# Kernel optimization log

Measured on AMD Instinct MI355X. Metric: run time of the kernel, lower is better.

## Reference

```python
import jax, jax.numpy as jnp
import numpy as np

N, E, G = 32768, 262144, 512
IN_DIM, HID, HEADS = 300, 128, 4
D_FUSED = HID * HEADS  # 512
L = 3


def setup_inputs() -> dict:
    key = jax.random.key(0)
    ks = jax.random.split(key, 24)
    s = 0.02
    inp = {
        "x": jax.random.normal(ks[0], (N, IN_DIM), jnp.float32),
        "edge_index": jax.random.randint(ks[1], (2, E), 0, N, jnp.int32),
        "batch": jnp.sort(jax.random.randint(ks[2], (N,), 0, G, jnp.int32)),
        "syn_w": jax.random.normal(ks[3], (IN_DIM, HID)) * s,
        "syn_b": jnp.zeros((HID,), jnp.float32),
        "ant_w": jax.random.normal(ks[4], (IN_DIM, HID)) * s,
        "ant_b": jnp.zeros((HID,), jnp.float32),
        "fusion_w": jax.random.normal(ks[5], (2 * HID, D_FUSED)) * s,
        "fusion_b": jnp.zeros((D_FUSED,), jnp.float32),
        "Wq": jax.random.normal(ks[6], (L, D_FUSED, D_FUSED)) * s,
        "bq": jnp.zeros((L, D_FUSED), jnp.float32),
        "Wk": jax.random.normal(ks[7], (L, D_FUSED, D_FUSED)) * s,
        "bk": jnp.zeros((L, D_FUSED), jnp.float32),
        "Wv": jax.random.normal(ks[8], (L, D_FUSED, D_FUSED)) * s,
        "bv": jnp.zeros((L, D_FUSED), jnp.float32),
        "Wskip": jax.random.normal(ks[9], (L, D_FUSED, D_FUSED)) * s,
        "bskip": jnp.zeros((L, D_FUSED), jnp.float32),
        "cls_w1": jax.random.normal(ks[10], (D_FUSED, HID)) * s,
        "cls_b1": jnp.zeros((HID,), jnp.float32),
        "cls_w2": jax.random.normal(ks[11], (HID, 1)) * s,
        "cls_b2": jnp.zeros((1,), jnp.float32),
    }
    return inp


def _transformer_conv(h, src, dst, Wq, bq, Wk, bk, Wv, bv, Wskip, bskip):
    # PyG TransformerConv: per-edge dot-product attention, softmax over in-neighbors of dst,
    # concat heads, plus root/skip linear (root_weight=True, concat=True, no edge_attr).
    n = h.shape[0]
    q = (h @ Wq + bq).reshape(n, HEADS, HID)
    k = (h @ Wk + bk).reshape(n, HEADS, HID)
    v = (h @ Wv + bv).reshape(n, HEADS, HID)
    scale = 1.0 / np.sqrt(HID)
    logits = jnp.einsum("ehd,ehd->eh", q[dst], k[src]) * scale  # [E, H]
    m = jax.ops.segment_max(logits, dst, num_segments=n)        # [N, H]
    e = jnp.exp(logits - m[dst])
    z = jax.ops.segment_sum(e, dst, num_segments=n)
    alpha = e / (z[dst] + 1e-16)                                # [E, H]
    msg = alpha[:, :, None] * v[src]                            # [E, H, D]
    out = jax.ops.segment_sum(msg, dst, num_segments=n).reshape(n, D_FUSED)
    return out + h @ Wskip + bskip


def reference(x, edge_index, batch, syn_w, syn_b, ant_w, ant_b, fusion_w, fusion_b,
              Wq, bq, Wk, bk, Wv, bv, Wskip, bskip, cls_w1, cls_b1, cls_w2, cls_b2):
    x_syn = jax.nn.relu(x @ syn_w + syn_b)
    x_ant = jax.nn.relu(x @ ant_w + ant_b)
    h = jnp.concatenate([x_syn, x_ant], axis=1) @ fusion_w + fusion_b  # [N, 512]
    src, dst = edge_index[0], edge_index[1]
    for l in range(L):
        h = jax.nn.relu(_transformer_conv(h, src, dst, Wq[l], bq[l], Wk[l], bk[l],
                                          Wv[l], bv[l], Wskip[l], bskip[l]))
    cnt = jax.ops.segment_sum(jnp.ones((h.shape[0],), h.dtype), batch, num_segments=G)
    pooled = jax.ops.segment_sum(h, batch, num_segments=G) / jnp.maximum(cnt, 1.0)[:, None]
    hid = jax.nn.relu(pooled @ cls_w1 + cls_b1)
    out = jax.nn.sigmoid(hid @ cls_w2 + cls_b2)
    return out.squeeze()
```

## Files before the change

kernel.cpp:

```cpp
#include <hip/hip_runtime.h>
#include <hip/hip_bf16.h>
#include <hip/hip_fp8.h>
#include <math.h>

#define N_NODES 32768
#define N_EDGES 262144
#define N_GRAPHS 512
#define IN_DIM 300
#define KPAD 320
#define HID 128
#define HEADS 4
#define D_FUSED 512
#define N_LAYERS 3

typedef __hip_bfloat16 bf16;
typedef short bf16x8 __attribute__((ext_vector_type(8)));
typedef float f32x4 __attribute__((ext_vector_type(4)));
typedef float f32x2 __attribute__((ext_vector_type(2)));

__device__ __forceinline__ float bfs_to_f(short s)
{
    unsigned u = ((unsigned)(unsigned short)s) << 16;
    return __builtin_bit_cast(float, u);
}

__device__ __forceinline__ short f_to_bfs(float v)
{
    return (short)__builtin_bit_cast(unsigned short, __float2bfloat16(v));
}

__device__ __forceinline__ void bf8_to_f32(bf16x8 v, float* f)
{
#pragma unroll
    for (int j = 0; j < 8; ++j) f[j] = bfs_to_f(v[j]);
}

__device__ __forceinline__ unsigned char f32_to_fp8(float v)
{
#if __has_builtin(__builtin_amdgcn_cvt_pk_fp8_f32)
    int p = __builtin_amdgcn_cvt_pk_fp8_f32(v, v, 0, false);
    return (unsigned char)(p & 0xff);
#else
    __hip_fp8_e4m3 t(v);
    return (unsigned char)t.__x;
#endif
}

__device__ __forceinline__ void fp8x8_to_f32(uint2 w, float* f)
{
#if __has_builtin(__builtin_amdgcn_cvt_pk_f32_fp8)
    f32x2 a = __builtin_amdgcn_cvt_pk_f32_fp8((int)w.x, false);
    f32x2 b = __builtin_amdgcn_cvt_pk_f32_fp8((int)w.x, true);
    f32x2 c = __builtin_amdgcn_cvt_pk_f32_fp8((int)w.y, false);
    f32x2 d = __builtin_amdgcn_cvt_pk_f32_fp8((int)w.y, true);
    f[0] = a.x; f[1] = a.y; f[2] = b.x; f[3] = b.y;
    f[4] = c.x; f[5] = c.y; f[6] = d.x; f[7] = d.y;
#else
    const unsigned char* p = (const unsigned char*)&w;
#pragma unroll
    for (int j = 0; j < 8; ++j) {
        __hip_fp8_e4m3 t;
        t.__x = (__hip_fp8_storage_t)p[j];
        f[j] = (float)t;
    }
#endif
}

__device__ __forceinline__ void gload_lds16(const void* g, void* l)
{
    __builtin_amdgcn_global_load_lds(
        (const __attribute__((address_space(1))) void*)g,
        (__attribute__((address_space(3))) void*)l, 16, 0, 0);
}

template <int K, int ACT, int EPI>
__global__ __launch_bounds__(512, 2) void mfma_gemm256(
    const bf16* __restrict__ A, int lda,
    const bf16* __restrict__ Bt,
    const float* __restrict__ bias,
    bf16* __restrict__ C0, int ldc0,
    bf16* __restrict__ C1, int ldc1, int csplit,
    unsigned char* __restrict__ C2,
    int nbx)
{
    __shared__ __align__(16) char lds[131072];

    const int t = threadIdx.x;
    const int wid = t >> 6, lane = t & 63;
    const int hi = lane >> 4, li = lane & 15;
    const int wr = wid >> 2, wc = wid & 3;

    int wg = blockIdx.x;
    if ((gridDim.x & 7) == 0) {
        const int cpx = gridDim.x >> 3;
        wg = (wg & 7) * cpx + (wg >> 3);
    }
    const int mb = wg / nbx, nb = wg % nbx;
    const int brow = mb * 256, bcol = nb * 256;
    constexpr int NT = K >> 6;

    const bf16* gA[4];
    const bf16* gB[4];
    int lbA[4], lbB[4];
#pragma unroll
    for (int j = 0; j < 4; ++j) {
        const int c = j * 512 + wid * 64 + lane;
        const int row = c >> 3;
        const int colb8 = ((c & 7) ^ (row & 7)) * 8;
        gA[j] = A + (size_t)(brow + row) * lda + colb8;
        gB[j] = Bt + (size_t)(bcol + row) * K + colb8;
        lbA[j] = (j * 512 + wid * 64) * 16;
        lbB[j] = 32768 + (j * 512 + wid * 64) * 16;
    }

    f32x4 acc[8][4] = {};

    auto stage = [&](int buf, int kt) {
        const int ko = kt * 64;
#pragma unroll
        for (int j = 0; j < 4; ++j)
            gload_lds16(gA[j] + ko, lds + buf * 65536 + lbA[j]);
#pragma unroll
        for (int j = 0; j < 4; ++j)
            gload_lds16(gB[j] + ko, lds + buf * 65536 + lbB[j]);
    };

    auto compute = [&](int b) {
        const char* Ab = lds + b * 65536;
        const char* Bb = Ab + 32768;
        bf16x8 bfrag[4][2];
#pragma unroll
        for (int n = 0; n < 4; ++n)
#pragma unroll
            for (int ks = 0; ks < 2; ++ks) {
                const int row = wc * 64 + n * 16 + li;
                bfrag[n][ks] = *(const bf16x8*)(
                    Bb + row * 128 + (((ks * 4 + hi) ^ (row & 7)) << 4));
            }
#pragma unroll
        for (int p = 0; p < 4; ++p) {
            bf16x8 afrag[2][2];
#pragma unroll
            for (int mm = 0; mm < 2; ++mm)
#pragma unroll
                for (int ks = 0; ks < 2; ++ks) {
                    const int row = wr * 128 + (p * 2 + mm) * 16 + li;
                    afrag[mm][ks] = *(const bf16x8*)(
                        Ab + row * 128 + (((ks * 4 + hi) ^ (row & 7)) << 4));
                }
            __builtin_amdgcn_s_setprio(1);
#pragma unroll
            for (int ks = 0; ks < 2; ++ks)
#pragma unroll
                for (int mm = 0; mm < 2; ++mm)
#pragma unroll
                    for (int n = 0; n < 4; ++n)
                        acc[p * 2 + mm][n] = __builtin_amdgcn_mfma_f32_16x16x32_bf16(
                            afrag[mm][ks], bfrag[n][ks], acc[p * 2 + mm][n], 0, 0, 0);
            __builtin_amdgcn_s_setprio(0);
        }
    };

    stage(0, 0);
#pragma unroll
    for (int kt = 0; kt < NT - 1; ++kt) {
        const int b = kt & 1;
        stage(b ^ 1, kt + 1);
        asm volatile("s_waitcnt vmcnt(8)" ::: "memory");
        __builtin_amdgcn_s_barrier();
        compute(b);
        asm volatile("" ::: "memory");
        __builtin_amdgcn_s_barrier();
    }
    asm volatile("s_waitcnt vmcnt(0)" ::: "memory");
    __builtin_amdgcn_s_barrier();
    compute((NT - 1) & 1);

#pragma unroll
    for (int m = 0; m < 8; ++m) {
#pragma unroll
        for (int n = 0; n < 4; ++n) {
            const int col = bcol + wc * 64 + n * 16 + li;
            const float bv = bias[col];
            if (EPI == 0) {
                const bool lo = (col < csplit);
                bf16* Cd = lo ? C0 : C1;
                const int ldc = lo ? ldc0 : ldc1;
                const int cc = lo ? col : col - csplit;
#pragma unroll
                for (int r = 0; r < 4; ++r) {
                    const int row = brow + wr * 128 + m * 16 + hi * 4 + r;
                    float v = acc[m][n][r] + bv;
                    if (ACT == 1) v = fmaxf(v, 0.f);
                    Cd[(size_t)row * ldc + cc] = __float2bfloat16(v);
                }
            } else {
#pragma unroll
                for (int r = 0; r < 4; ++r) {
                    const int row = brow + wr * 128 + m * 16 + hi * 4 + r;
                    const float v = acc[m][n][r] + bv;
                    if (col < 512) {
                        C0[(size_t)row * ldc0 + col] = __float2bfloat16(v);
                    } else if (col < 1024) {
                        C1[(size_t)row * ldc1 + (col - 512)] = __float2bfloat16(v);
                    } else {
                        C2[(size_t)row * 1024 + (col - 1024)] = f32_to_fp8(v);
                    }
                }
            }
        }
    }
}

template <int ACT>
__global__ __launch_bounds__(256) void mfma_gemm(
    const bf16* __restrict__ A, int lda,
    const bf16* __restrict__ Bt,
    const float* __restrict__ bias,
    bf16* __restrict__ C, int ldc, int K)
{
    __shared__ __align__(16) char lds[16384];
    char* As = lds;
    char* Bs = lds + 8192;

    const int t = threadIdx.x;
    const int wid = t >> 6, lane = t & 63;
    const int brow = blockIdx.x * 128;
    const int bcol = blockIdx.y * 128;
    const int wr = wid >> 1, wc = wid & 1;

    f32x4 acc[4][4] = {};

    for (int k0 = 0; k0 < K; k0 += 32) {
#pragma unroll
        for (int j = 0; j < 2; ++j) {
            const int seg = wid * 2 + j;
            const int row = seg * 16 + (lane >> 2);
            const int clin = lane & 3;
            const int clog = clin ^ ((row >> 1) & 3);
            gload_lds16(A + (size_t)(brow + row) * lda + k0 + clog * 8,
                        As + seg * 1024);
            gload_lds16(Bt + (size_t)(bcol + row) * K + k0 + clog * 8,
                        Bs + seg * 1024);
        }
        __syncthreads();

        bf16x8 af[4], bfr[4];
#pragma unroll
        for (int m = 0; m < 4; ++m) {
            const int row = wr * 64 + m * 16 + (lane & 15);
            const int cl = (lane >> 4) ^ ((row >> 1) & 3);
            af[m] = *(const bf16x8*)(As + row * 64 + cl * 16);
        }
#pragma unroll
        for (int n = 0; n < 4; ++n) {
            const int row = wc * 64 + n * 16 + (lane & 15);
            const int cl = (lane >> 4) ^ ((row >> 1) & 3);
            bfr[n] = *(const bf16x8*)(Bs + row * 64 + cl * 16);
        }
#pragma unroll
        for (int m = 0; m < 4; ++m)
#pragma unroll
            for (int n = 0; n < 4; ++n)
                acc[m][n] = __builtin_amdgcn_mfma_f32_16x16x32_bf16(
                    af[m], bfr[n], acc[m][n], 0, 0, 0);
        __syncthreads();
    }

#pragma unroll
    for (int m = 0; m < 4; ++m) {
#pragma unroll
        for (int n = 0; n < 4; ++n) {
            const int col = bcol + wc * 64 + n * 16 + (lane & 15);
            const float bv = bias[col];
#pragma unroll
            for (int r = 0; r < 4; ++r) {
                const int row = brow + wr * 64 + m * 16 + (lane >> 4) * 4 + r;
                float v = acc[m][n][r] + bv;
                if (ACT == 1) v = fmaxf(v, 0.f);
                C[(size_t)row * ldc + col] = __float2bfloat16(v);
            }
        }
    }
}

__global__ void prep_xpad_kernel(const float* __restrict__ x, bf16* __restrict__ xb)
{
    const int n = blockIdx.x, k = threadIdx.x;
    xb[(size_t)n * KPAD + k] =
        __float2bfloat16(k < IN_DIM ? x[(size_t)n * IN_DIM + k] : 0.f);
}

__global__ void prep_encw_kernel(const float* __restrict__ syn_w,
                                 const float* __restrict__ ant_w,
                                 bf16* __restrict__ wt)
{
    const int c = blockIdx.x, k = threadIdx.x;
    float v = 0.f;
    if (k < IN_DIM) v = (c < HID) ? syn_w[k * HID + c] : ant_w[k * HID + (c - HID)];
    wt[c * KPAD + k] = __float2bfloat16(v);
}

__global__ void prep_fusw_kernel(const float* __restrict__ fw, bf16* __restrict__ wt)
{
    const int c = blockIdx.x, k = threadIdx.x;
    wt[c * 256 + k] = __float2bfloat16(fw[k * D_FUSED + c]);
}

__global__ __launch_bounds__(256) void prep_combw_kernel(
    const float* __restrict__ Wskip,
    const float* __restrict__ Wq,
    const float* __restrict__ Wk,
    const float* __restrict__ Wv,
    bf16* __restrict__ wt)
{
    __shared__ float tile[32][33];
    const int blk = blockIdx.x;
    const int l = blk >> 10, rem = blk & 1023;
    const int cb = rem >> 4, kb = rem & 15;
    const int c0 = cb * 32;

    const int sel = c0 >> 9;
    const float* mat = (sel == 0) ? Wskip : (sel == 1) ? Wq : (sel == 2) ? Wk : Wv;
    const int cp0 = c0 & 511;

    const int j = threadIdx.x & 31;
    const int i0 = threadIdx.x >> 5;
#pragma unroll
    for (int s = 0; s < 4; ++s) {
        const int i = i0 + 8 * s;
        tile[i][j] = mat[((size_t)l * 512 + kb * 32 + i) * 512 + cp0 + j];
    }
    __syncthreads();
#pragma unroll
    for (int s = 0; s < 4; ++s) {
        const int jj = i0 + 8 * s;
        wt[((size_t)l * 2048 + c0 + jj) * 512 + kb * 32 + j] =
            __float2bfloat16(tile[j][jj]);
    }
}

__global__ void prep_bias_kernel(const float* __restrict__ syn_b,
                                 const float* __restrict__ ant_b,
                                 const float* __restrict__ bskip,
                                 const float* __restrict__ bq,
                                 const float* __restrict__ bk,
                                 const float* __restrict__ bv,
                                 float* __restrict__ benc,
                                 float* __restrict__ bcomb)
{
    const int i = blockIdx.x * 256 + threadIdx.x;
    if (i < 256) benc[i] = (i < HID) ? syn_b[i] : ant_b[i - HID];
    const int j = i - 256;
    if (j >= 0 && j < 6144) {
        const int l = j >> 11, c = j & 2047;
        const int sel = c >> 9, col = c & 511;
        const float* s = (sel == 0) ? bskip : (sel == 1) ? bq : (sel == 2) ? bk : bv;
        bcomb[j] = s[l * D_FUSED + col];
    }
}

__global__ void zero_int_kernel(int* __restrict__ p, int n)
{
    int i = blockIdx.x * 256 + threadIdx.x;
    if (i < n) p[i] = 0;
}

__global__ void hist_kernel(const int* __restrict__ dst, int* __restrict__ deg, int E)
{
    int e = blockIdx.x * 256 + threadIdx.x;
    if (e < E) atomicAdd(&deg[dst[e]], 1);
}

__global__ __launch_bounds__(256) void partial_sum_kernel(const int* __restrict__ deg,
                                                          int* __restrict__ part)
{
    int v = deg[blockIdx.x * 256 + threadIdx.x];
#pragma unroll
    for (int o = 32; o; o >>= 1) v += __shfl_xor(v, o);
    __shared__ int w4[4];
    if ((threadIdx.x & 63) == 0) w4[threadIdx.x >> 6] = v;
    __syncthreads();
    if (threadIdx.x == 0) part[blockIdx.x] = w4[0] + w4[1] + w4[2] + w4[3];
}

__global__ __launch_bounds__(128) void scan_part_kernel(int* __restrict__ part)
{
    __shared__ int s[128];
    const int t = threadIdx.x;
    s[t] = part[t];
    __syncthreads();
    for (int o = 1; o < 128; o <<= 1) {
        int v = (t >= o) ? s[t - o] : 0;
        __syncthreads();
        s[t] += v;
        __syncthreads();
    }
    part[t] = (t == 0) ? 0 : s[t - 1];
}

__global__ __launch_bounds__(256) void off_kernel(const int* __restrict__ deg,
                                                  const int* __restrict__ part,
                                                  int* __restrict__ off)
{
    __shared__ int s[256];
    const int b = blockIdx.x, t = threadIdx.x;
    s[t] = deg[b * 256 + t];
    __syncthreads();
    for (int o = 1; o < 256; o <<= 1) {
        int v = (t >= o) ? s[t - o] : 0;
        __syncthreads();
        s[t] += v;
        __syncthreads();
    }
    const int excl = (t == 0) ? 0 : s[t - 1];
    off[b * 256 + t] = part[b] + excl;
    if (b == 127 && t == 255) off[N_NODES] = part[127] + s[255];
}

__global__ void scatter_kernel(const int* __restrict__ src, const int* __restrict__ dst,
                               const int* __restrict__ off, int* __restrict__ cursor,
                               int* __restrict__ csr_src, int E)
{
    int e = blockIdx.x * 256 + threadIdx.x;
    if (e < E) {
        int d = dst[e];
        int pos = atomicAdd(&cursor[d], 1);
        csr_src[off[d] + pos] = src[e];
    }
}

__global__ __launch_bounds__(256) void attn_kernel(
    const bf16* __restrict__ qb, const unsigned char* __restrict__ kvb,
    bf16* __restrict__ hout, const int* __restrict__ off,
    const int* __restrict__ csr)
{
    const int n = blockIdx.x;
    const int hd = threadIdx.x >> 6;
    const int lane = threadIdx.x & 63;
    const int g = lane >> 4, sub = lane & 15;
    const float scale = 0.08838834764831845f;

    float qf[8];
    bf8_to_f32(*(const bf16x8*)(qb + (size_t)n * 512 + hd * 128 + sub * 8), qf);

    float m = -1e30f, z = 0.f;
    float acc[8] = {};

    const int s0 = off[n], s1 = off[n + 1];
    for (int e0 = s0; e0 < s1; e0 += 4) {
        const int e = e0 + g;
        const bool valid = (e < s1);
        const int srcn = valid ? csr[e] : 0;
        const unsigned char* kp = kvb + (size_t)srcn * 1024 + hd * 128 + sub * 8;

        float kf[8];
        fp8x8_to_f32(*(const uint2*)kp, kf);
        float d = 0.f;
#pragma unroll
        for (int j = 0; j < 8; ++j) d = fmaf(qf[j], kf[j], d);
        d += __shfl_xor(d, 1);
        d += __shfl_xor(d, 2);
        d += __shfl_xor(d, 4);
        d += __shfl_xor(d, 8);

        const float logit = d * scale;
        const float mn = valid ? fmaxf(m, logit) : m;
        const float corr = __expf(m - mn);
        const float w = valid ? __expf(logit - mn) : 0.f;
        z = z * corr + w;

        float vf[8];
        fp8x8_to_f32(*(const uint2*)(kp + 512), vf);
#pragma unroll
        for (int j = 0; j < 8; ++j) acc[j] = acc[j] * corr + w * vf[j];
        m = mn;
    }

    float mm = fmaxf(m, __shfl_xor(m, 16));
    mm = fmaxf(mm, __shfl_xor(mm, 32));
    const float f = __expf(m - mm);
    float zz = z * f;
    zz += __shfl_xor(zz, 16);
    zz += __shfl_xor(zz, 32);
    const float inv = 1.f / (zz + 1e-16f);

    float o[8];
#pragma unroll
    for (int j = 0; j < 8; ++j) {
        float a = acc[j] * f;
        a += __shfl_xor(a, 16);
        a += __shfl_xor(a, 32);
        o[j] = a * inv;
    }

    if (g == 0) {
        const size_t ob = (size_t)n * D_FUSED + hd * HID + sub * 8;
        const bf16x8 sk = *(const bf16x8*)(hout + ob);
        bf16x8 res;
#pragma unroll
        for (int j = 0; j < 8; ++j)
            res[j] = f_to_bfs(fmaxf(o[j] + bfs_to_f(sk[j]), 0.f));
        *(bf16x8*)(hout + ob) = res;
    }
}

__global__ __launch_bounds__(256) void pool_kernel(const bf16* __restrict__ h,
                                                   const int* __restrict__ batch,
                                                   float* __restrict__ pooled)
{
    const int g = blockIdx.x;
    int a = 0, b = N_NODES;
    while (a < b) { int mid = (a + b) >> 1; if (batch[mid] < g) a = mid + 1; else b = mid; }
    const int start = a;
    b = N_NODES;
    while (a < b) { int mid = (a + b) >> 1; if (batch[mid] < g + 1) a = mid + 1; else b = mid; }
    const int end = a;
    const float invc = 1.f / fmaxf((float)(end - start), 1.f);

    const int t = threadIdx.x;
    float2 s = make_float2(0.f, 0.f);
    for (int nidx = start; nidx < end; ++nidx) {
        const bf16* p = h + (size_t)nidx * D_FUSED + t * 2;
        s.x += bfs_to_f(((const short*)p)[0]);
        s.y += bfs_to_f(((const short*)p)[1]);
    }
    pooled[(size_t)g * D_FUSED + t * 2]     = s.x * invc;
    pooled[(size_t)g * D_FUSED + t * 2 + 1] = s.y * invc;
}

__global__ __launch_bounds__(128) void cls_kernel(const float* __restrict__ pooled,
                                                  const float* __restrict__ w1,
                                                  const float* __restrict__ b1,
                                                  const float* __restrict__ w2,
                                                  const float* __restrict__ b2,
                                                  float* __restrict__ out)
{
    const int g = blockIdx.x;
    const int j = threadIdx.x;
    const float* p = pooled + (size_t)g * D_FUSED;
    float acc = 0.f;
    for (int i = 0; i < D_FUSED; ++i) acc += p[i] * w1[i * HID + j];
    const float hid = fmaxf(acc + b1[j], 0.f);
    float val = hid * w2[j];
#pragma unroll
    for (int o = 32; o; o >>= 1) val += __shfl_xor(val, o);
    __shared__ float ws2[2];
    if ((threadIdx.x & 63) == 0) ws2[threadIdx.x >> 6] = val;
    __syncthreads();
    if (threadIdx.x == 0) {
        const float sum = ws2[0] + ws2[1] + b2[0];
        out[g] = 1.f / (1.f + __expf(-sum));
    }
}

extern "C" void kernel_launch(void* const* d_in, const int* in_sizes, int n_in,
                              void* d_out, int out_size, void* d_ws, size_t ws_size,
                              hipStream_t stream)
{
    const float* x        = (const float*)d_in[0];
    const int*   ei       = (const int*)d_in[1];
    const int*   batch    = (const int*)d_in[2];
    const float* syn_w    = (const float*)d_in[3];
    const float* syn_b    = (const float*)d_in[4];
    const float* ant_w    = (const float*)d_in[5];
    const float* ant_b    = (const float*)d_in[6];
    const float* fusion_w = (const float*)d_in[7];
    const float* fusion_b = (const float*)d_in[8];
    const float* Wq       = (const float*)d_in[9];
    const float* bq       = (const float*)d_in[10];
    const float* Wk       = (const float*)d_in[11];
    const float* bk       = (const float*)d_in[12];
    const float* Wv       = (const float*)d_in[13];
    const float* bv       = (const float*)d_in[14];
    const float* Wskip    = (const float*)d_in[15];
    const float* bskip    = (const float*)d_in[16];
    const float* cls_w1   = (const float*)d_in[17];
    const float* cls_b1   = (const float*)d_in[18];
    const float* cls_w2   = (const float*)d_in[19];
    const float* cls_b2   = (const float*)d_in[20];

    const int* src = ei;
    const int* dst = ei + N_EDGES;

    const size_t NV = (size_t)N_NODES * D_FUSED;
    bf16* hA    = (bf16*)d_ws;
    bf16* hB    = hA + NV;
    bf16* qbuf  = hB + NV;
    unsigned char* kvbuf = (unsigned char*)(qbuf + NV);
    bf16* wenc  = (bf16*)(kvbuf + (size_t)N_NODES * 1024);
    bf16* wfus  = wenc + 256 * KPAD;
    bf16* wcomb = wfus + 512 * 256;
    float* benc = (float*)(wcomb + (size_t)3 * 2048 * 512);
    float* bcomb = benc + 256;
    float* pooled = bcomb + 6144;
    int* deg    = (int*)(pooled + (size_t)N_GRAPHS * D_FUSED);
    int* cursor = deg + N_NODES;
    int* part   = cursor + N_NODES;
    int* off    = part + 128;
    int* csr    = off + N_NODES + 1;

    bf16* xb   = qbuf;
    bf16* tenc = hB;

    zero_int_kernel<<<(2 * N_NODES + 255) / 256, 256, 0, stream>>>(deg, 2 * N_NODES);
    hist_kernel<<<N_EDGES / 256, 256, 0, stream>>>(dst, deg, N_EDGES);
    partial_sum_kernel<<<128, 256, 0, stream>>>(deg, part);
    scan_part_kernel<<<1, 128, 0, stream>>>(part);
    off_kernel<<<128, 256, 0, stream>>>(deg, part, off);
    scatter_kernel<<<N_EDGES / 256, 256, 0, stream>>>(src, dst, off, cursor, csr, N_EDGES);

    prep_xpad_kernel<<<N_NODES, KPAD, 0, stream>>>(x, xb);
    prep_encw_kernel<<<256, KPAD, 0, stream>>>(syn_w, ant_w, wenc);
    prep_fusw_kernel<<<512, 256, 0, stream>>>(fusion_w, wfus);
    prep_combw_kernel<<<3072, 256, 0, stream>>>(Wskip, Wq, Wk, Wv, wcomb);
    prep_bias_kernel<<<25, 256, 0, stream>>>(syn_b, ant_b, bskip, bq, bk, bv, benc, bcomb);

    mfma_gemm<1><<<dim3(N_NODES / 128, 2), 256, 0, stream>>>(
        xb, KPAD, wenc, benc, tenc, 256, KPAD);
    mfma_gemm256<256, 0, 0><<<256, 512, 0, stream>>>(
        tenc, 256, wfus, fusion_b, hA, D_FUSED, hA, D_FUSED, D_FUSED, nullptr, 2);

    bf16* hcur = hA;
    bf16* hnew = hB;
    for (int l = 0; l < N_LAYERS; ++l) {
        mfma_gemm256<512, 0, 1><<<1024, 512, 0, stream>>>(
            hcur, D_FUSED, wcomb + (size_t)l * 2048 * D_FUSED,
            bcomb + (size_t)l * 2048,
            hnew, D_FUSED, qbuf, D_FUSED, 512, kvbuf, 8);
        attn_kernel<<<N_NODES, 256, 0, stream>>>(qbuf, kvbuf, hnew, off, csr);
        bf16* tmp = hcur; hcur = hnew; hnew = tmp;
    }

    pool_kernel<<<N_GRAPHS, 256, 0, stream>>>(hcur, batch, pooled);
    cls_kernel<<<N_GRAPHS, 128, 0, stream>>>(pooled, cls_w1, cls_b1, cls_w2, cls_b2,
                                             (float*)d_out);
}
```

Baseline: 647.6 us.

## Interleave next-tile global-to-LDS loads with MFMA phases in GEMM main loop

Restructures the 256x256 bf16 GEMM main loop so the prefetch of the next K tile is split into four parts, each issued between the MFMA phases of the current tile. Barriers are added around each phase, and the LDS layout is reorganized into 128-row slabs. The goal is to spread memory traffic across the compute and keep the issue pattern balanced, in the style of ping-pong scheduling. The extra barriers per phase add synchronization cost and could stall waves.

Result: no change. 654.3 us (+1.0%).

```diff
diff --git a/kernel.cpp b/kernel.cpp
--- a/kernel.cpp
+++ b/kernel.cpp
@@ -99,55 +99,72 @@
     const int brow = mb * 256, bcol = nb * 256;
     constexpr int NT = K >> 6;
 
-    const bf16* gA[4];
-    const bf16* gB[4];
-    int lbA[4], lbB[4];
-#pragma unroll
-    for (int j = 0; j < 4; ++j) {
-        const int c = j * 512 + wid * 64 + lane;
-        const int row = c >> 3;
-        const int colb8 = ((c & 7) ^ (row & 7)) * 8;
-        gA[j] = A + (size_t)(brow + row) * lda + colb8;
-        gB[j] = Bt + (size_t)(bcol + row) * K + colb8;
-        lbA[j] = (j * 512 + wid * 64) * 16;
-        lbB[j] = 32768 + (j * 512 + wid * 64) * 16;
-    }
+    const int row0 = t >> 3, sl0 = (((t & 7) ^ (row0 & 7)) * 8);
+    const int c1i = t + 512;
+    const int row1 = c1i >> 3, sl1 = (((c1i & 7) ^ (row1 & 7)) * 8);
+
+    const bf16* srcs[4][2];
+    srcs[0][0] = A  + (size_t)(brow + row0)       * lda + sl0;
+    srcs[0][1] = A  + (size_t)(brow + row1)       * lda + sl1;
+    srcs[1][0] = A  + (size_t)(brow + 128 + row0) * lda + sl0;
+    srcs[1][1] = A  + (size_t)(brow + 128 + row1) * lda + sl1;
+    srcs[2][0] = Bt + (size_t)(bcol + row0)       * K   + sl0;
+    srcs[2][1] = Bt + (size_t)(bcol + row1)       * K   + sl1;
+    srcs[3][0] = Bt + (size_t)(bcol + 128 + row0) * K   + sl0;
+    srcs[3][1] = Bt + (size_t)(bcol + 128 + row1) * K   + sl1;
+
+    auto stage_part = [&](int buf, int kt1, int q) {
+        const int ko = kt1 * 64;
+        const int slab = buf * 65536 + (q >> 1) * 32768 + (q & 1) * 16384;
+        gload_lds16(srcs[q][0] + ko, lds + slab + wid * 1024);
+        gload_lds16(srcs[q][1] + ko, lds + slab + 8192 + wid * 1024);
+    };
 
     f32x4 acc[8][4] = {};
 
-    auto stage = [&](int buf, int kt) {
-        const int ko = kt * 64;
-#pragma unroll
-        for (int j = 0; j < 4; ++j)
-            gload_lds16(gA[j] + ko, lds + buf * 65536 + lbA[j]);
-#pragma unroll
-        for (int j = 0; j < 4; ++j)
-            gload_lds16(gB[j] + ko, lds + buf * 65536 + lbB[j]);
-    };
-
-    auto compute = [&](int b) {
-        const char* Ab = lds + b * 65536;
-        const char* Bb = Ab + 32768;
+#pragma unroll
+    for (int q = 0; q < 4; ++q) stage_part(0, 0, q);
+
+#pragma unroll
+    for (int kt = 0; kt < NT; ++kt) {
+        const int b = kt & 1;
+        const char* Aslab = lds + b * 65536 + wr * 16384;
+        const char* Bslab = lds + b * 65536 + 32768 + (wc >> 1) * 16384;
+        const int bRow0 = (wc & 1) * 64;
+
+        if (kt < NT - 1) {
+            stage_part(b ^ 1, kt + 1, 0);
+            asm volatile("s_waitcnt vmcnt(2)" ::: "memory");
+        } else {
+            asm volatile("s_waitcnt vmcnt(0)" ::: "memory");
+        }
+        __builtin_amdgcn_s_barrier();
+        __builtin_amdgcn_sched_barrier(0);
+
         bf16x8 bfrag[4][2];
 #pragma unroll
-        for (int n = 0; n < 4; ++n)
-#pragma unroll
-            for (int ks = 0; ks < 2; ++ks) {
-                const int row = wc * 64 + n * 16 + li;
-                bfrag[n][ks] = *(const bf16x8*)(
-                    Bb + row * 128 + (((ks * 4 + hi) ^ (row & 7)) << 4));
+        for (int q = 0; q < 4; ++q) {
+            if (q > 0 && kt < NT - 1) stage_part(b ^ 1, kt + 1, q);
+            if (q == 0) {
+#pragma unroll
+                for (int n = 0; n < 4; ++n)
+#pragma unroll
+                    for (int ks = 0; ks < 2; ++ks) {
+                        const int row = bRow0 + n * 16 + li;
+                        bfrag[n][ks] = *(const bf16x8*)(
+                            Bslab + row * 128 + (((ks * 4 + hi) ^ (row & 7)) << 4));
+                    }
             }
-#pragma unroll
-        for (int p = 0; p < 4; ++p) {
-            bf16x8 afrag[2][2];
+            bf16x8 af[2][2];
 #pragma unroll
             for (int mm = 0; mm < 2; ++mm)
 #pragma unroll
                 for (int ks = 0; ks < 2; ++ks) {
-                    const int row = wr * 128 + (p * 2 + mm) * 16 + li;
-                    afrag[mm][ks] = *(const bf16x8*)(
-                        Ab + row * 128 + (((ks * 4 + hi) ^ (row & 7)) << 4));
+                    const int row = (q * 2 + mm) * 16 + li;
+                    af[mm][ks] = *(const bf16x8*)(
+                        Aslab + row * 128 + (((ks * 4 + hi) ^ (row & 7)) << 4));
                 }
+            __builtin_amdgcn_s_barrier();
             __builtin_amdgcn_s_setprio(1);
 #pragma unroll
             for (int ks = 0; ks < 2; ++ks)
@@ -155,26 +172,12 @@
                 for (int mm = 0; mm < 2; ++mm)
 #pragma unroll
                     for (int n = 0; n < 4; ++n)
-                        acc[p * 2 + mm][n] = __builtin_amdgcn_mfma_f32_16x16x32_bf16(
-                            afrag[mm][ks], bfrag[n][ks], acc[p * 2 + mm][n], 0, 0, 0);
+                        acc[q * 2 + mm][n] = __builtin_amdgcn_mfma_f32_16x16x32_bf16(
+                            af[mm][ks], bfrag[n][ks], acc[q * 2 + mm][n], 0, 0, 0);
             __builtin_amdgcn_s_setprio(0);
+            __builtin_amdgcn_s_barrier();
         }
-    };
-
-    stage(0, 0);
-#pragma unroll
-    for (int kt = 0; kt < NT - 1; ++kt) {
-        const int b = kt & 1;
-        stage(b ^ 1, kt + 1);
-        asm volatile("s_waitcnt vmcnt(8)" ::: "memory");
-        __builtin_amdgcn_s_barrier();
-        compute(b);
-        asm volatile("" ::: "memory");
-        __builtin_amdgcn_s_barrier();
-    }
-    asm volatile("s_waitcnt vmcnt(0)" ::: "memory");
-    __builtin_amdgcn_s_barrier();
-    compute((NT - 1) & 1);
+    }
 
 #pragma unroll
     for (int m = 0; m < 8; ++m) {
```
